# Optimization experiments

Hardware: AMD Instinct MI355X
Metric: run time of the kernel (lower is better)

Reference implementation:

```python
import jax, jax.numpy as jnp
import numpy as np

B, T, E_A, E_B, E_ATT, N_HEAD = 2, 2048, 2048, 2048, 2048, 16
HS = E_ATT // N_HEAD  # 128
ROPE_BASE = 100000.0


def setup_inputs() -> dict:
    key = jax.random.key(0)
    ks = jax.random.split(key, 6)
    Ta = T // 2
    x_a = jax.random.normal(ks[0], (B, Ta, E_A), jnp.float32)
    x_b = jax.random.normal(ks[1], (B, T - Ta, E_B), jnp.float32)
    # alternating text/other tokens: even positions are stream-a
    mask_a = jnp.tile((jnp.arange(T) % 2 == 0)[None, :], (B, 1))
    # standard RoPE tables, full head_size (freqs duplicated), as litgpt/nanoGPT build them
    pos = jnp.arange(T, dtype=jnp.float32)
    inv_freq = 1.0 / (ROPE_BASE ** (jnp.arange(0, HS, 2, dtype=jnp.float32) / HS))
    freqs = pos[:, None] * inv_freq[None, :]           # [T, HS/2]
    emb = jnp.concatenate([freqs, freqs], axis=-1)      # [T, HS]
    cos, sin = jnp.cos(emb), jnp.sin(emb)
    s = 0.02
    Wqkv_a = jax.random.normal(ks[2], (E_A, 3 * E_ATT), jnp.float32) * s
    Wqkv_b = jax.random.normal(ks[3], (E_B, 3 * E_ATT), jnp.float32) * s
    Wproj_a = jax.random.normal(ks[4], (E_ATT, E_A), jnp.float32) * s
    Wproj_b = jax.random.normal(ks[5], (E_ATT, E_B), jnp.float32) * s
    return dict(x_a=x_a, x_b=x_b, cos=cos, sin=sin, mask_a=mask_a,
                Wqkv_a=Wqkv_a, Wqkv_b=Wqkv_b, Wproj_a=Wproj_a, Wproj_b=Wproj_b)


def _apply_rope(x, cos, sin):
    # x: [B, H, T, HS]; cos/sin: [T, HS] broadcast over leading dims
    x1 = x[..., : HS // 2]
    x2 = x[..., HS // 2:]
    rot = jnp.concatenate([-x2, x1], axis=-1)
    return (x * cos + rot * sin).astype(x.dtype)


def reference(x_a, x_b, cos, sin, mask_a, Wqkv_a, Wqkv_b, Wproj_a, Wproj_b):
    Bm, Tm = mask_a.shape
    Na = x_a.shape[0] * x_a.shape[1]  # static token counts per stream
    Nb = x_b.shape[0] * x_b.shape[1]
    C3 = Wqkv_a.shape[1]              # 3 * E_ATT
    # dual-stream QKV projections (bias=False)
    qkv_a = (x_a @ Wqkv_a).reshape(-1, C3)
    qkv_b = (x_b @ Wqkv_b).reshape(-1, C3)
    # interleave tokens back into the full [B, T] layout by mask scatter
    flat = mask_a.reshape(-1)
    idx_a = jnp.nonzero(flat, size=Na)[0]
    idx_b = jnp.nonzero(~flat, size=Nb)[0]
    kqv = jnp.zeros((Bm * Tm, C3), qkv_a.dtype).at[idx_a].set(qkv_a).at[idx_b].set(qkv_b)
    kqv = kqv.reshape(Bm, Tm, 3 * N_HEAD, HS).transpose(0, 2, 1, 3)  # [B, 3H, T, hs]
    q, k, v = kqv[:, :N_HEAD], kqv[:, N_HEAD:2 * N_HEAD], kqv[:, 2 * N_HEAD:]
    q = _apply_rope(q, cos, sin)
    k = _apply_rope(k, cos, sin)
    # causal SDPA (dropout_p = 0 at eval)
    scale = 1.0 / np.sqrt(HS).astype(np.float32)
    att = jnp.einsum('bhqd,bhkd->bhqk', q, k) * scale
    causal = jnp.tril(jnp.ones((Tm, Tm), bool))
    att = jnp.where(causal, att, -jnp.inf)
    att = jax.nn.softmax(att, axis=-1)
    y = jnp.einsum('bhqk,bhkd->bhqd', att, v)
    y = y.transpose(0, 2, 1, 3).reshape(Bm * Tm, N_HEAD * HS)
    # mask split + per-stream output projections
    y_a = y[idx_a] @ Wproj_a
    y_b = y[idx_b] @ Wproj_b
    return (y_a, y_b)
```

## Files before the change

kernel.cpp:

```cpp
#include <hip/hip_runtime.h>
#include <hip/hip_bf16.h>


typedef __attribute__((ext_vector_type(8))) short v8s;
typedef __attribute__((ext_vector_type(4))) float v4f;

#define GL2LDS(gptr, lptr)                                              \
  __builtin_amdgcn_global_load_lds(                                     \
      (const __attribute__((address_space(1))) void*)(gptr),            \
      (__attribute__((address_space(3))) void*)(lptr), 16, 0, 0)

#define S_BARRIER() asm volatile("s_barrier" ::: "memory")

__device__ __forceinline__ float b2f(unsigned short u) {
  return __uint_as_float(((unsigned int)u) << 16);
}
__device__ __forceinline__ unsigned short f2bf(float f) {
  unsigned int u = __float_as_uint(f);
  u += 0x7fffu + ((u >> 16) & 1u);
  return (unsigned short)(u >> 16);
}

__global__ __launch_bounds__(256) void f32_to_bf16_2(
    const float4* __restrict__ a, const float4* __restrict__ b,
    uint2* __restrict__ out, int n4each) {
  int i = blockIdx.x * 256 + threadIdx.x;
  if (i >= 2 * n4each) return;
  float4 v = (i < n4each) ? a[i] : b[i - n4each];
  uint2 o;
  o.x = (unsigned int)f2bf(v.x) | ((unsigned int)f2bf(v.y) << 16);
  o.y = (unsigned int)f2bf(v.z) | ((unsigned int)f2bf(v.w) << 16);
  out[i] = o;
}

__global__ __launch_bounds__(256) void transpose_f32_bf16(
    const float* __restrict__ in0, const float* __restrict__ in1,
    unsigned short* __restrict__ out0, unsigned short* __restrict__ out1,
    int R, int C) {
  const float* in = blockIdx.z ? in1 : in0;
  unsigned short* out = blockIdx.z ? out1 : out0;
  __shared__ unsigned short tile[64][65];
  const int bc = blockIdx.x * 64, br = blockIdx.y * 64;
  const int c  = threadIdx.x & 63;
  const int r0 = threadIdx.x >> 6;
  for (int r = r0; r < 64; r += 4)
    tile[r][c] = f2bf(in[(size_t)(br + r) * C + bc + c]);
  __syncthreads();
  for (int rr = r0; rr < 64; rr += 4)
    out[(size_t)(bc + rr) * R + br + c] = tile[c][rr];
}

template <int MH, int NH>
__device__ __forceinline__ void mfma_quad(v4f (&acc)[8][4], const v8s (&a)[4][2],
                                          const v8s (&b)[4][2]) {
  __builtin_amdgcn_s_setprio(1);
#pragma unroll
  for (int ks = 0; ks < 2; ++ks)
#pragma unroll
    for (int i = 0; i < 4; ++i)
#pragma unroll
      for (int j = 0; j < 2; ++j)
        acc[MH * 4 + i][NH * 2 + j] = __builtin_amdgcn_mfma_f32_16x16x32_bf16(
            a[i][ks], b[NH * 2 + j][ks], acc[MH * 4 + i][NH * 2 + j], 0, 0, 0);
  __builtin_amdgcn_s_setprio(0);
}

__device__ __forceinline__ void read_a_half(const unsigned short* lds, int base,
                                            int mh, int r, int c0, int c1,
                                            v8s (&a)[4][2]) {
#pragma unroll
  for (int i = 0; i < 4; ++i) {
    const unsigned short* ap = lds + base + (mh * 64 + i * 16 + r) * 64;
    a[i][0] = *(const v8s*)(ap + c0);
    a[i][1] = *(const v8s*)(ap + c1);
  }
}

template <int NH>
__device__ __forceinline__ void read_b_half(const unsigned short* lds, int base,
                                            int brow, int r, int c0, int c1,
                                            v8s (&b)[4][2]) {
#pragma unroll
  for (int j = 0; j < 2; ++j) {
    const unsigned short* bp = lds + base + (brow + (NH * 2 + j) * 16 + r) * 64;
    b[NH * 2 + j][0] = *(const v8s*)(bp + c0);
    b[NH * 2 + j][1] = *(const v8s*)(bp + c1);
  }
}

template <int GATHER, int OSCAT>
__global__ __launch_bounds__(512, 2) void gemm256(
    const unsigned short* __restrict__ A,
    const unsigned short* __restrict__ BT0,
    const unsigned short* __restrict__ BT1,
    void* __restrict__ Cout, int M, int N, int K, int NBN) {
  __shared__ __align__(16) unsigned short lds[65536];
  const int tid = threadIdx.x;
  const int par = blockIdx.y;
  const unsigned short* __restrict__ BT = par ? BT1 : BT0;

  int wg = blockIdx.x;
  const int cpx = gridDim.x >> 3;
  wg = (wg & 7) * cpx + (wg >> 3);
  const int m0 = (wg / NBN) * 256, n0 = (wg % NBN) * 256;

  const int w = tid >> 6, lane = tid & 63;
  const int wm = w >> 2, wn = w & 3;
  const int r = lane & 15, q = lane >> 4;
  const int rs = r & 7;
  const int c0 = ((q ^ rs) << 3);
  const int c1 = (((4 + q) ^ rs) << 3);
  const int brow = (wn & 1) << 6;
  const int AbaseE = (2 + wm) * 8192, BbaseE = (wn >> 1) * 8192;
  const int AbaseO = (6 + wm) * 8192, BbaseO = (4 + (wn >> 1)) * 8192;

  const int sr0 = tid >> 3, sslot = tid & 7;
  const int NT = K >> 6, NIT = NT >> 1;

  auto stageB = [&](int p, int tt) {
    unsigned short* dst = &lds[(((tt << 2) + p) & 7) * 8192 + w * 512];
#pragma unroll
    for (int cc = 0; cc < 2; ++cc) {
      const int row = sr0 + cc * 64;
      const int g = ((sslot ^ (row & 7)) << 3);
      GL2LDS(BT + (size_t)(n0 + p * 128 + row) * K + tt * 64 + g, dst + cc * 4096);
    }
  };
  auto stageA = [&](int p, int tt) {
    unsigned short* dst = &lds[(((tt << 2) + 2 + p) & 7) * 8192 + w * 512];
#pragma unroll
    for (int cc = 0; cc < 2; ++cc) {
      const int row = sr0 + cc * 64;
      const int g = ((sslot ^ (row & 7)) << 3);
      int ar = m0 + p * 128 + row;
      if constexpr (GATHER) ar = ((ar >> 10) << 11) + ((ar & 1023) << 1) + par;
      GL2LDS(A + (size_t)ar * K + tt * 64 + g, dst + cc * 4096);
    }
  };

  v4f acc[8][4] = {};
  v8s a[4][2], b[4][2];

  stageB(0, 0); stageB(1, 0); stageA(0, 0); stageA(1, 0);
  asm volatile("" ::: "memory");
  stageB(0, 1); stageB(1, 1);
  asm volatile("s_waitcnt vmcnt(4)" ::: "memory");
  S_BARRIER();

  for (int it = 0; it < NIT; ++it) {
    const int t = it << 1;
    const bool more = (it + 1 < NIT);

    read_a_half(lds, AbaseE, 0, r, c0, c1, a);
    read_b_half<0>(lds, BbaseE, brow, r, c0, c1, b);
    stageA(0, t + 1);
    S_BARRIER();
    mfma_quad<0, 0>(acc, a, b);
    S_BARRIER();
    read_b_half<1>(lds, BbaseE, brow, r, c0, c1, b);
    stageA(1, t + 1);
    S_BARRIER();
    mfma_quad<0, 1>(acc, a, b);
    S_BARRIER();
    read_a_half(lds, AbaseE, 1, r, c0, c1, a);
    if (more) stageB(0, t + 2);
    S_BARRIER();
    mfma_quad<1, 0>(acc, a, b);
    S_BARRIER();
    if (more) stageB(1, t + 2);
    S_BARRIER();
    mfma_quad<1, 1>(acc, a, b);
    if (more) { asm volatile("s_waitcnt vmcnt(4)" ::: "memory"); }
    else      { asm volatile("s_waitcnt vmcnt(0)" ::: "memory"); }
    S_BARRIER();

    read_a_half(lds, AbaseO, 0, r, c0, c1, a);
    read_b_half<0>(lds, BbaseO, brow, r, c0, c1, b);
    if (more) stageA(0, t + 2);
    S_BARRIER();
    mfma_quad<0, 0>(acc, a, b);
    S_BARRIER();
    read_b_half<1>(lds, BbaseO, brow, r, c0, c1, b);
    if (more) stageA(1, t + 2);
    S_BARRIER();
    mfma_quad<0, 1>(acc, a, b);
    S_BARRIER();
    read_a_half(lds, AbaseO, 1, r, c0, c1, a);
    if (more) stageB(0, t + 3);
    S_BARRIER();
    mfma_quad<1, 0>(acc, a, b);
    S_BARRIER();
    if (more) stageB(1, t + 3);
    S_BARRIER();
    mfma_quad<1, 1>(acc, a, b);
    if (more) { asm volatile("s_waitcnt vmcnt(4)" ::: "memory"); }
    S_BARRIER();
  }

  float* Cf = (float*)Cout + (size_t)par * M * N;
  unsigned short* Cb = (unsigned short*)Cout;
#pragma unroll
  for (int tm = 0; tm < 8; ++tm) {
    const int rowm = m0 + wm * 128 + tm * 16 + q * 4;
#pragma unroll
    for (int tn = 0; tn < 4; ++tn) {
      const int col = n0 + wn * 64 + tn * 16 + r;
#pragma unroll
      for (int p = 0; p < 4; ++p) {
        if constexpr (OSCAT == 0) {
          Cf[(size_t)(rowm + p) * N + col] = acc[tm][tn][p];
        } else {
          const int ar = rowm + p;
          const int orow = ((ar >> 10) << 11) + ((ar & 1023) << 1) + (OSCAT - 1);
          Cb[(size_t)orow * N + col] = f2bf(acc[tm][tn][p]);
        }
      }
    }
  }
}

__global__ __launch_bounds__(256) void scatter_rope(
    const unsigned short* __restrict__ qkv,
    const float* __restrict__ cosb, const float* __restrict__ sinb,
    unsigned short* __restrict__ Q, unsigned short* __restrict__ K) {
  const int token = blockIdx.x;
  const int b = token >> 11, t = token & 2047;
  const unsigned short* src = qkv + (size_t)token * 6144;
  for (int i = threadIdx.x; i < 2048; i += 256) {
    const int d = i & 127, h = i >> 7;
    const float cv = cosb[t * 128 + d];
    const float sv = sinb[t * 128 + d];
    const int   mate = (d < 64) ? i + 64 : i - 64;
    const float sgn  = (d < 64) ? -1.f : 1.f;
    const float qv = b2f(src[i]),        qm = b2f(src[mate]) * sgn;
    const float kv = b2f(src[2048 + i]), km = b2f(src[2048 + mate]) * sgn;
    const size_t off = ((size_t)(b * 16 + h) * 2048 + t) * 128 + d;
    Q[off] = f2bf(qv * cv + qm * sv);
    K[off] = f2bf(kv * cv + km * sv);
  }
}

__global__ __launch_bounds__(256) void transpose_v(
    const unsigned short* __restrict__ qkv, unsigned short* __restrict__ Vt) {
  __shared__ unsigned short tile[128][129];
  const int bh = blockIdx.x >> 4, tt = blockIdx.x & 15;
  const int b = bh >> 4, h = bh & 15;
  const int tid = threadIdx.x;
  const int d0 = tid & 127, t0 = tid >> 7;
#pragma unroll 4
  for (int i = 0; i < 64; ++i) {
    int tl = i * 2 + t0;
    tile[tl][d0] =
        qkv[((size_t)(b * 2048 + tt * 128 + tl)) * 6144 + 4096 + h * 128 + d0];
  }
  __syncthreads();
#pragma unroll 4
  for (int i = 0; i < 64; ++i) {
    int dd = i * 2 + t0;
    Vt[((size_t)(bh * 128 + dd)) * 2048 + tt * 128 + d0] = tile[d0][dd];
  }
}

#define SIG 0.1275174038536989f

__global__ __launch_bounds__(256, 2) void attn_flash(
    const unsigned short* __restrict__ Q, const unsigned short* __restrict__ K,
    const unsigned short* __restrict__ Vt, unsigned short* __restrict__ Y) {
  __shared__ __align__(16) unsigned short Ks[64 * 128];
  __shared__ __align__(16) unsigned short Vs[128 * 64];
  __shared__ __align__(16) unsigned short QP[64 * 128];

  const int bh = blockIdx.x >> 4, pr = blockIdx.x & 15;
  const int tid = threadIdx.x, w = tid >> 6, lane = tid & 63;
  const int r = lane & 15, q = lane >> 4;
  const int b = bh >> 4, h = bh & 15;
  const size_t kbase = (size_t)bh * 2048 * 128;
  const size_t vbase = (size_t)bh * 128 * 2048;

  for (int ph = 0; ph < 2; ++ph) {
    const int qt = ph ? pr : (31 - pr);

    const size_t qbase = ((size_t)bh * 2048 + qt * 64) * 128;
#pragma unroll
    for (int i = 0; i < 4; ++i) {
      const int rowl = w * 16 + i * 4 + q;
      const int g = r ^ (rowl & 15);
      GL2LDS(Q + qbase + (size_t)rowl * 128 + g * 8, &QP[(w * 16 + i * 4) * 128]);
    }
    __builtin_amdgcn_s_waitcnt(0);
    v8s qf[4];
#pragma unroll
    for (int ki = 0; ki < 4; ++ki) {
      const int rowl = w * 16 + r;
      const int c = (ki * 4 + q) ^ r;
      qf[ki] = *(const v8s*)&QP[rowl * 128 + c * 8];
    }
    __syncthreads();

    float mrun[4], lrun[4];
    v4f O[8] = {};
#pragma unroll
    for (int p = 0; p < 4; ++p) { mrun[p] = -3.0e38f; lrun[p] = 0.f; }

    const int nkt = qt + 1;
    for (int kt = 0; kt < nkt; ++kt) {
#pragma unroll
      for (int i = 0; i < 4; ++i) {
        const int key = w * 16 + i * 4 + q;
        const int g = r ^ (key & 15);
        GL2LDS(K + kbase + ((size_t)kt * 64 + key) * 128 + g * 8,
               &Ks[(w * 16 + i * 4) * 128]);
      }
      const int vrow = lane >> 3, pc = lane & 7;
#pragma unroll
      for (int i = 0; i < 4; ++i) {
        const int d = w * 32 + i * 8 + vrow;
        const int g = pc ^ (d & 7);
        GL2LDS(Vt + vbase + (size_t)d * 2048 + kt * 64 + g * 8,
               &Vs[(w * 32 + i * 8) * 64]);
      }
      __builtin_amdgcn_s_waitcnt(0);
      __syncthreads();

      v4f S[4] = {};
#pragma unroll
      for (int ki = 0; ki < 4; ++ki) {
        v8s kf[4];
#pragma unroll
        for (int tn = 0; tn < 4; ++tn) {
          const int key = tn * 16 + r;
          const int c = (ki * 4 + q) ^ r;
          kf[tn] = *(const v8s*)&Ks[key * 128 + c * 8];
        }
#pragma unroll
        for (int tn = 0; tn < 4; ++tn)
          S[tn] = __builtin_amdgcn_mfma_f32_16x16x32_bf16(
              qf[ki], kf[tn], S[tn], 0, 0, 0);
      }

      if (kt == qt) {
#pragma unroll
        for (int tn = 0; tn < 4; ++tn)
#pragma unroll
          for (int p = 0; p < 4; ++p) {
            const int tq = w * 16 + q * 4 + p;
            const int kg = tn * 16 + r;
            if (kg > tq) S[tn][p] = -3.0e38f;
          }
      }

#pragma unroll
      for (int p = 0; p < 4; ++p) {
        float mx = fmaxf(fmaxf(S[0][p], S[1][p]), fmaxf(S[2][p], S[3][p]));
#pragma unroll
        for (int o = 1; o < 16; o <<= 1) mx = fmaxf(mx, __shfl_xor(mx, o, 64));
        const float mnew = fmaxf(mrun[p], mx);
        const float alpha = exp2f((mrun[p] - mnew) * SIG);
        mrun[p] = mnew;
        float sum = 0.f;
#pragma unroll
        for (int tn = 0; tn < 4; ++tn) {
          const float pv = exp2f((S[tn][p] - mnew) * SIG);
          S[tn][p] = pv;
          sum += pv;
        }
#pragma unroll
        for (int o = 1; o < 16; o <<= 1) sum += __shfl_xor(sum, o, 64);
        lrun[p] = lrun[p] * alpha + sum;
#pragma unroll
        for (int tn = 0; tn < 8; ++tn) O[tn][p] *= alpha;
      }

#pragma unroll
      for (int tn = 0; tn < 4; ++tn)
#pragma unroll
        for (int p = 0; p < 4; ++p) {
          const int m = w * 16 + q * 4 + p;
          QP[m * 72 + tn * 16 + r] = f2bf(S[tn][p]);
        }

#pragma unroll
      for (int ki = 0; ki < 2; ++ki) {
        v8s pf, vf[8];
        const int m = w * 16 + r;
        pf = *(const v8s*)&QP[m * 72 + (ki * 4 + q) * 8];
#pragma unroll
        for (int tn = 0; tn < 8; ++tn) {
          const int d = tn * 16 + r;
          const int c = (ki * 4 + q) ^ (d & 7);
          vf[tn] = *(const v8s*)&Vs[d * 64 + c * 8];
        }
#pragma unroll
        for (int tn = 0; tn < 8; ++tn)
          O[tn] = __builtin_amdgcn_mfma_f32_16x16x32_bf16(
              pf, vf[tn], O[tn], 0, 0, 0);
      }
      __syncthreads();
    }

#pragma unroll
    for (int p = 0; p < 4; ++p) {
      const float inv = 1.0f / lrun[p];
      const int t = qt * 64 + w * 16 + q * 4 + p;
#pragma unroll
      for (int tn = 0; tn < 8; ++tn)
        Y[((size_t)(b * 2048 + t)) * 2048 + h * 128 + tn * 16 + r] =
            f2bf(O[tn][p] * inv);
    }
  }
}

extern "C" void kernel_launch(void* const* d_in, const int* in_sizes, int n_in,
                              void* d_out, int out_size, void* d_ws, size_t ws_size,
                              hipStream_t stream) {
  const float* x_a   = (const float*)d_in[0];
  const float* x_b   = (const float*)d_in[1];
  const float* cosb  = (const float*)d_in[2];
  const float* sinb  = (const float*)d_in[3];
  const float* Wqkv_a  = (const float*)d_in[5];
  const float* Wqkv_b  = (const float*)d_in[6];
  const float* Wproj_a = (const float*)d_in[7];
  const float* Wproj_b = (const float*)d_in[8];
  float* out = (float*)d_out;

  if (ws_size < 100663296u) return;

  char* ws = (char*)d_ws;
  unsigned short* QKVall = (unsigned short*)(ws);
  unsigned short* XA     = (unsigned short*)(ws + 50331648);
  unsigned short* WQT    = (unsigned short*)(ws + 67108864);
  unsigned short* Qb     = (unsigned short*)(ws + 50331648);
  unsigned short* Kb     = (unsigned short*)(ws + 67108864);
  unsigned short* Vtb    = (unsigned short*)(ws + 83886080);
  unsigned short* Yb     = (unsigned short*)(ws);
  unsigned short* WPT_A  = (unsigned short*)(ws + 16777216);
  unsigned short* WPT_B  = (unsigned short*)(ws + 25165824);

  hipLaunchKernelGGL(f32_to_bf16_2, dim3(8192), dim3(256), 0, stream,
                     (const float4*)x_a, (const float4*)x_b, (uint2*)XA, 1048576);
  hipLaunchKernelGGL(transpose_f32_bf16, dim3(96, 32, 1), dim3(256), 0, stream,
                     Wqkv_a, Wqkv_a, WQT, WQT, 2048, 6144);
  hipLaunchKernelGGL((gemm256<0, 1>), dim3(192, 1), dim3(512), 0, stream,
                     XA, WQT, WQT, QKVall, 2048, 6144, 2048, 24);
  hipLaunchKernelGGL(transpose_f32_bf16, dim3(96, 32, 1), dim3(256), 0, stream,
                     Wqkv_b, Wqkv_b, WQT, WQT, 2048, 6144);
  hipLaunchKernelGGL((gemm256<0, 2>), dim3(192, 1), dim3(512), 0, stream,
                     XA + (size_t)4194304, WQT, WQT, QKVall, 2048, 6144, 2048, 24);

  hipLaunchKernelGGL(scatter_rope, dim3(4096), dim3(256), 0, stream,
                     QKVall, cosb, sinb, Qb, Kb);
  hipLaunchKernelGGL(transpose_v, dim3(512), dim3(256), 0, stream,
                     QKVall, Vtb);

  hipLaunchKernelGGL(transpose_f32_bf16, dim3(32, 32, 2), dim3(256), 0, stream,
                     Wproj_a, Wproj_b, WPT_A, WPT_B, 2048, 2048);

  hipLaunchKernelGGL(attn_flash, dim3(512), dim3(256), 0, stream,
                     Qb, Kb, Vtb, Yb);

  hipLaunchKernelGGL((gemm256<1, 0>), dim3(64, 2), dim3(512), 0, stream,
                     Yb, WPT_A, WPT_B, out, 2048, 2048, 2048, 8);
}
```

Baseline: 497.8 us.

## Double-buffer K/V tiles in flash attention and prefetch the next tile

The attention kernel now keeps two LDS buffers for K and V. It issues the global-to-LDS loads for tile kt+1 before computing on tile kt and waits with a partial vmcnt, so memory latency overlaps the MFMA work. Q fragments are read straight from global memory instead of being staged through LDS. The block index is remapped so that neighbouring blocks span different heads, and s_setprio brackets the MFMA sections. The extra buffers roughly double the LDS footprint, which may limit the two-blocks-per-CU occupancy, and the hand-written waitcnt and barrier sequence must stay correct.

```diff
diff --git a/kernel.cpp b/kernel.cpp
--- a/kernel.cpp
+++ b/kernel.cpp
@@ -266,36 +266,29 @@
 __global__ __launch_bounds__(256, 2) void attn_flash(
     const unsigned short* __restrict__ Q, const unsigned short* __restrict__ K,
     const unsigned short* __restrict__ Vt, unsigned short* __restrict__ Y) {
-  __shared__ __align__(16) unsigned short Ks[64 * 128];
-  __shared__ __align__(16) unsigned short Vs[128 * 64];
-  __shared__ __align__(16) unsigned short QP[64 * 128];
-
-  const int bh = blockIdx.x >> 4, pr = blockIdx.x & 15;
+  __shared__ __align__(16) unsigned short Ks[2][64 * 128];
+  __shared__ __align__(16) unsigned short Vs[2][128 * 64];
+  __shared__ __align__(16) unsigned short Pl[64 * 72];
+
+  const int x = blockIdx.x;
+  const int bh = (x & 7) * 4 + ((x >> 3) & 3);
+  const int pr = x >> 5;
   const int tid = threadIdx.x, w = tid >> 6, lane = tid & 63;
   const int r = lane & 15, q = lane >> 4;
   const int b = bh >> 4, h = bh & 15;
   const size_t kbase = (size_t)bh * 2048 * 128;
   const size_t vbase = (size_t)bh * 128 * 2048;
+  const int vrow = lane >> 3, pc = lane & 7;
 
   for (int ph = 0; ph < 2; ++ph) {
     const int qt = ph ? pr : (31 - pr);
 
     const size_t qbase = ((size_t)bh * 2048 + qt * 64) * 128;
-#pragma unroll
-    for (int i = 0; i < 4; ++i) {
-      const int rowl = w * 16 + i * 4 + q;
-      const int g = r ^ (rowl & 15);
-      GL2LDS(Q + qbase + (size_t)rowl * 128 + g * 8, &QP[(w * 16 + i * 4) * 128]);
-    }
-    __builtin_amdgcn_s_waitcnt(0);
     v8s qf[4];
 #pragma unroll
-    for (int ki = 0; ki < 4; ++ki) {
-      const int rowl = w * 16 + r;
-      const int c = (ki * 4 + q) ^ r;
-      qf[ki] = *(const v8s*)&QP[rowl * 128 + c * 8];
-    }
-    __syncthreads();
+    for (int ki = 0; ki < 4; ++ki)
+      qf[ki] = *(const v8s*)&Q[qbase + (size_t)(w * 16 + r) * 128 +
+                               (ki * 4 + q) * 8];
 
     float mrun[4], lrun[4];
     v4f O[8] = {};
@@ -303,26 +296,37 @@
     for (int p = 0; p < 4; ++p) { mrun[p] = -3.0e38f; lrun[p] = 0.f; }
 
     const int nkt = qt + 1;
-    for (int kt = 0; kt < nkt; ++kt) {
+
+    auto stageKV = [&](int kt, int buf) {
 #pragma unroll
       for (int i = 0; i < 4; ++i) {
         const int key = w * 16 + i * 4 + q;
-        const int g = r ^ (key & 15);
-        GL2LDS(K + kbase + ((size_t)kt * 64 + key) * 128 + g * 8,
-               &Ks[(w * 16 + i * 4) * 128]);
-      }
-      const int vrow = lane >> 3, pc = lane & 7;
+        const int gs = r ^ (key & 15);
+        GL2LDS(K + kbase + ((size_t)kt * 64 + key) * 128 + gs * 8,
+               &Ks[buf][(w * 16 + i * 4) * 128]);
+      }
 #pragma unroll
       for (int i = 0; i < 4; ++i) {
         const int d = w * 32 + i * 8 + vrow;
-        const int g = pc ^ (d & 7);
-        GL2LDS(Vt + vbase + (size_t)d * 2048 + kt * 64 + g * 8,
-               &Vs[(w * 32 + i * 8) * 64]);
-      }
-      __builtin_amdgcn_s_waitcnt(0);
-      __syncthreads();
+        const int gs = pc ^ (d & 7);
+        GL2LDS(Vt + vbase + (size_t)d * 2048 + kt * 64 + gs * 8,
+               &Vs[buf][(w * 32 + i * 8) * 64]);
+      }
+    };
+
+    stageKV(0, 0);
+    for (int kt = 0; kt < nkt; ++kt) {
+      const int buf = kt & 1;
+      if (kt + 1 < nkt) {
+        stageKV(kt + 1, buf ^ 1);
+        asm volatile("s_waitcnt vmcnt(8)" ::: "memory");
+      } else {
+        asm volatile("s_waitcnt vmcnt(0)" ::: "memory");
+      }
+      S_BARRIER();
 
       v4f S[4] = {};
+      __builtin_amdgcn_s_setprio(1);
 #pragma unroll
       for (int ki = 0; ki < 4; ++ki) {
         v8s kf[4];
@@ -330,13 +334,14 @@
         for (int tn = 0; tn < 4; ++tn) {
           const int key = tn * 16 + r;
           const int c = (ki * 4 + q) ^ r;
-          kf[tn] = *(const v8s*)&Ks[key * 128 + c * 8];
+          kf[tn] = *(const v8s*)&Ks[buf][key * 128 + c * 8];
         }
 #pragma unroll
         for (int tn = 0; tn < 4; ++tn)
           S[tn] = __builtin_amdgcn_mfma_f32_16x16x32_bf16(
               qf[ki], kf[tn], S[tn], 0, 0, 0);
       }
+      __builtin_amdgcn_s_setprio(0);
 
       if (kt == qt) {
 #pragma unroll
@@ -376,26 +381,30 @@
 #pragma unroll
         for (int p = 0; p < 4; ++p) {
           const int m = w * 16 + q * 4 + p;
-          QP[m * 72 + tn * 16 + r] = f2bf(S[tn][p]);
+          Pl[m * 72 + tn * 16 + r] = f2bf(S[tn][p]);
         }
 
+      __builtin_amdgcn_s_setprio(1);
 #pragma unroll
       for (int ki = 0; ki < 2; ++ki) {
         v8s pf, vf[8];
         const int m = w * 16 + r;
-        pf = *(const v8s*)&QP[m * 72 + (ki * 4 + q) * 8];
+        pf = *(const v8s*)&Pl[m * 72 + (ki * 4 + q) * 8];
 #pragma unroll
         for (int tn = 0; tn < 8; ++tn) {
           const int d = tn * 16 + r;
           const int c = (ki * 4 + q) ^ (d & 7);
-          vf[tn] = *(const v8s*)&Vs[d * 64 + c * 8];
+          vf[tn] = *(const v8s*)&Vs[buf][d * 64 + c * 8];
         }
 #pragma unroll
         for (int tn = 0; tn < 8; ++tn)
           O[tn] = __builtin_amdgcn_mfma_f32_16x16x32_bf16(
               pf, vf[tn], O[tn], 0, 0, 0);
       }
-      __syncthreads();
+      __builtin_amdgcn_s_setprio(0);
+
+      asm volatile("s_waitcnt lgkmcnt(0)" ::: "memory");
+      S_BARRIER();
     }
 
 #pragma unroll
```

After: 495.9 us. Within noise of the previous version (-0.4%).
